# Optimization experiments

Measured on AMD Instinct MI355X. Metric: run time of the kernel, lower is better.

Reference implementation:

```python
import jax, jax.numpy as jnp
import numpy as np

NUM_EDGE_TYPES = 8
HIDDEN = 128
N_NODES = 50000
N_EDGES = 600000


def setup_inputs() -> dict:
    key = jax.random.key(0)
    ks = jax.random.split(key, 10)
    H = HIDDEN
    h = jax.random.normal(ks[0], (N_NODES, H), dtype=jnp.float32)
    edge_index = jax.random.randint(ks[1], (2, N_EDGES), 0, N_NODES, dtype=jnp.int32)
    edge_type = jax.random.randint(ks[2], (N_EDGES,), 0, NUM_EDGE_TYPES + 1, dtype=jnp.int32)
    s = 1.0 / np.sqrt(H)
    W_msg = jax.random.uniform(ks[3], (H, H), jnp.float32, -s, s)
    b_msg = jax.random.uniform(ks[4], (H,), jnp.float32, -s, s)
    edge_embed = jax.random.normal(ks[5], (NUM_EDGE_TYPES + 1, H), dtype=jnp.float32)
    W_ih = jax.random.uniform(ks[6], (3 * H, H), jnp.float32, -s, s)
    W_hh = jax.random.uniform(ks[7], (3 * H, H), jnp.float32, -s, s)
    b_ih = jax.random.uniform(ks[8], (3 * H,), jnp.float32, -s, s)
    b_hh = jax.random.uniform(ks[9], (3 * H,), jnp.float32, -s, s)
    return {"h": h, "edge_index": edge_index, "edge_type": edge_type,
            "num_nodes": N_NODES, "W_msg": W_msg, "b_msg": b_msg,
            "edge_embed": edge_embed, "W_ih": W_ih, "W_hh": W_hh,
            "b_ih": b_ih, "b_hh": b_hh}


def _gru_cell(x, h, W_ih, W_hh, b_ih, b_hh):
    # PyTorch GRUCell: gates ordered (r, z, n)
    H = h.shape[-1]
    gi = x @ W_ih.T + b_ih  # (N, 3H)
    gh = h @ W_hh.T + b_hh
    i_r, i_z, i_n = gi[:, :H], gi[:, H:2 * H], gi[:, 2 * H:]
    h_r, h_z, h_n = gh[:, :H], gh[:, H:2 * H], gh[:, 2 * H:]
    r = jax.nn.sigmoid(i_r + h_r)
    z = jax.nn.sigmoid(i_z + h_z)
    n = jnp.tanh(i_n + r * h_n)
    return (1.0 - z) * n + z * h


def reference(h, edge_index, edge_type, num_nodes, W_msg, b_msg, edge_embed, W_ih, W_hh, b_ih, b_hh):
    src = edge_index[0]
    dst = edge_index[1]
    # gather -> linear -> edge-type embed add
    src_h = h[src] @ W_msg.T + b_msg                      # (E, H)
    emb = edge_embed[jnp.clip(edge_type, 0, NUM_EDGE_TYPES)]  # (E, H)
    msg = src_h + emb
    # scatter-add into per-node message buffer
    messages = jax.ops.segment_sum(msg, dst, num_segments=num_nodes)  # (num_nodes, H)
    h_new = _gru_cell(messages, h[:num_nodes], W_ih, W_hh, b_ih, b_hh)
    result = jnp.zeros_like(h).at[:num_nodes].set(h_new)
    return result
```

## Files before the change

kernel.cpp:

```cpp
#include <hip/hip_runtime.h>
#include <math.h>

#define H 128
typedef unsigned int u32;
typedef unsigned long long u64;
typedef __attribute__((ext_vector_type(8))) short short8;
typedef __attribute__((ext_vector_type(4))) float floatx4;

#define XS_STRIDE 136
#define CS_STRIDE 40

__device__ __forceinline__ float sigmoid_f(float x) {
    return 1.0f / (1.0f + __expf(-x));
}
__device__ __forceinline__ float tanh_f(float x) {
    float t = __expf(-2.0f * fabsf(x));
    float r = (1.0f - t) / (1.0f + t);
    return copysignf(r, x);
}
__device__ __forceinline__ unsigned short f2bf(float x) {
    u32 u = __float_as_uint(x);
    return (unsigned short)((u + 0x7fffu + ((u >> 16) & 1u)) >> 16);
}
__device__ __forceinline__ float bf2f(unsigned short s) {
    return __uint_as_float(((u32)s) << 16);
}
__device__ __forceinline__ float bf_lo32(u32 u) { return __uint_as_float(u << 16); }
__device__ __forceinline__ float bf_hi32(u32 u) { return __uint_as_float(u & 0xffff0000u); }

__global__ __launch_bounds__(256) void fused_pre_kernel(
    const float* __restrict__ h, unsigned short* __restrict__ h_b, int total8,
    int* __restrict__ head, int N,
    const float* __restrict__ Wih, const float* __restrict__ Whh,
    const float* __restrict__ Wm,  const float* __restrict__ emb,
    const float* __restrict__ bm,
    unsigned short* __restrict__ Wcs, unsigned short* __restrict__ Whhs,
    unsigned short* __restrict__ embWs, int HB, int DB)
{
    int b = blockIdx.x;
    if (b < HB) {
        int idx = b * 256 + threadIdx.x;
        if (idx >= total8) return;
        const float4* p = (const float4*)(h + (size_t)idx * 8);
        float4 a = p[0], bb = p[1];
        short8 v;
        v[0] = (short)f2bf(a.x);  v[1] = (short)f2bf(a.y);
        v[2] = (short)f2bf(a.z);  v[3] = (short)f2bf(a.w);
        v[4] = (short)f2bf(bb.x); v[5] = (short)f2bf(bb.y);
        v[6] = (short)f2bf(bb.z); v[7] = (short)f2bf(bb.w);
        *(short8*)(h_b + (size_t)idx * 8) = v;
        return;
    }
    if (b < HB + DB) {
        int idx = (b - HB) * 256 + threadIdx.x;
        if (idx < N) head[idx] = -1;
        return;
    }
    int idx = (b - HB - DB) * 256 + threadIdx.x;
    if (idx < 49152) {
        int g = idx >> 7;
        int k = idx & 127;
        float acc = 0.f;
#pragma unroll 4
        for (int c = 0; c < H; ++c)
            acc += Wih[(size_t)g * H + c] * Wm[(size_t)c * H + k];
        int gate = g >> 7;
        int wi = g & 127;
        int j = wi >> 4, m = wi & 15;
        int kc = k >> 5, q = (k >> 3) & 3, i = k & 7;
        int l = q * 16 + m;
        Wcs[(size_t)(((gate * 8 + j) * 4 + kc) * 64 + l) * 8 + i] = f2bf(acc);
    } else if (idx < 61440) {
        int s = idx - 49152;
        int i = s & 7;
        int l = (s >> 3) & 63;
        int jb = s >> 9;
        int gate = jb >> 3, jj = jb & 7;
        int q = l >> 4, m = l & 15;
        int t = q * 8 + i;
        unsigned short v = 0;
        if (t < 9) {
            int g = gate * 128 + jj * 16 + m;
            float acc = 0.f;
#pragma unroll 4
            for (int jx = 0; jx < H; ++jx)
                acc += (emb[(size_t)t * H + jx] + bm[jx]) * Wih[(size_t)g * H + jx];
            v = f2bf(acc);
        }
        embWs[s] = v;
    } else if (idx < 67584) {
        int t2 = idx - 61440;
        int l  = t2 & 63;
        int kc = (t2 >> 6) & 3;
        int jr = t2 >> 8;
        int m = l & 15, q = l >> 4;
        size_t srco = (size_t)(jr * 16 + m) * H + kc * 32 + q * 8;
        const float4* s0 = (const float4*)(Whh + srco);
        float4 a = s0[0], bb = s0[1];
        short8 v;
        v[0] = (short)f2bf(a.x);  v[1] = (short)f2bf(a.y);
        v[2] = (short)f2bf(a.z);  v[3] = (short)f2bf(a.w);
        v[4] = (short)f2bf(bb.x); v[5] = (short)f2bf(bb.y);
        v[6] = (short)f2bf(bb.z); v[7] = (short)f2bf(bb.w);
        *(short8*)(Whhs + (size_t)t2 * 8) = v;
    }
}

__global__ __launch_bounds__(256) void fill_ll_kernel(
    const int* __restrict__ eidx, const int* __restrict__ etype,
    int* __restrict__ head, int* __restrict__ nexte,
    int* __restrict__ packed, int E)
{
    int e = blockIdx.x * 256 + threadIdx.x;
    if (e >= E) return;
    int src = eidx[e];
    int dst = eidx[E + e];
    int t = etype[e];
    t = t < 0 ? 0 : (t > 8 ? 8 : t);
    packed[e] = src | (t << 24);
    int old = atomicExch(&head[dst], e);
    nexte[e] = old;
}

__global__ __launch_bounds__(256) void gather_ll_kernel(
    const unsigned short* __restrict__ h_b,
    const int* __restrict__ head, const int* __restrict__ nexte,
    const int* __restrict__ packed,
    unsigned short* __restrict__ S_b, u64* __restrict__ cnt, int N)
{
    int w = blockIdx.x * 4 + (threadIdx.x >> 6);
    int lane = threadIdx.x & 63;
    int n0 = w * 4;
    if (n0 >= N) return;

    int e0 = head[n0];
    int e1 = (n0 + 1 < N) ? head[n0 + 1] : -1;
    int e2 = (n0 + 2 < N) ? head[n0 + 2] : -1;
    int e3 = (n0 + 3 < N) ? head[n0 + 3] : -1;

    float ax0 = 0.f, ay0 = 0.f, ax1 = 0.f, ay1 = 0.f;
    float ax2 = 0.f, ay2 = 0.f, ax3 = 0.f, ay3 = 0.f;
    u64 c0 = 0, c1 = 0, c2 = 0, c3 = 0;

    while ((e0 >= 0) || (e1 >= 0) || (e2 >= 0) || (e3 >= 0)) {
        int nx0 = -1, nx1 = -1, nx2 = -1, nx3 = -1;
        int u0 = 0, u1 = 0, u2 = 0, u3 = 0;
        if (e0 >= 0) { nx0 = nexte[e0]; u0 = packed[e0]; }
        if (e1 >= 0) { nx1 = nexte[e1]; u1 = packed[e1]; }
        if (e2 >= 0) { nx2 = nexte[e2]; u2 = packed[e2]; }
        if (e3 >= 0) { nx3 = nexte[e3]; u3 = packed[e3]; }
        if (e0 >= 0) {
            u32 x = *((const u32*)(h_b + (size_t)(u0 & 0xffffff) * H) + lane);
            c0 += 1ull << (7 * (u0 >> 24));
            ax0 += bf_lo32(x); ay0 += bf_hi32(x);
        }
        if (e1 >= 0) {
            u32 x = *((const u32*)(h_b + (size_t)(u1 & 0xffffff) * H) + lane);
            c1 += 1ull << (7 * (u1 >> 24));
            ax1 += bf_lo32(x); ay1 += bf_hi32(x);
        }
        if (e2 >= 0) {
            u32 x = *((const u32*)(h_b + (size_t)(u2 & 0xffffff) * H) + lane);
            c2 += 1ull << (7 * (u2 >> 24));
            ax2 += bf_lo32(x); ay2 += bf_hi32(x);
        }
        if (e3 >= 0) {
            u32 x = *((const u32*)(h_b + (size_t)(u3 & 0xffffff) * H) + lane);
            c3 += 1ull << (7 * (u3 >> 24));
            ax3 += bf_lo32(x); ay3 += bf_hi32(x);
        }
        e0 = nx0; e1 = nx1; e2 = nx2; e3 = nx3;
    }

    {
        u32 o = (u32)f2bf(ax0) | ((u32)f2bf(ay0) << 16);
        *((u32*)(S_b + (size_t)n0 * H) + lane) = o;
        if (lane == 0) cnt[n0] = c0;
    }
    if (n0 + 1 < N) {
        u32 o = (u32)f2bf(ax1) | ((u32)f2bf(ay1) << 16);
        *((u32*)(S_b + (size_t)(n0 + 1) * H) + lane) = o;
        if (lane == 0) cnt[n0 + 1] = c1;
    }
    if (n0 + 2 < N) {
        u32 o = (u32)f2bf(ax2) | ((u32)f2bf(ay2) << 16);
        *((u32*)(S_b + (size_t)(n0 + 2) * H) + lane) = o;
        if (lane == 0) cnt[n0 + 2] = c2;
    }
    if (n0 + 3 < N) {
        u32 o = (u32)f2bf(ax3) | ((u32)f2bf(ay3) << 16);
        *((u32*)(S_b + (size_t)(n0 + 3) * H) + lane) = o;
        if (lane == 0) cnt[n0 + 3] = c3;
    }
}

__global__ __launch_bounds__(256, 4) void gru_mfma_kernel(
    const unsigned short* __restrict__ S_b, const unsigned short* __restrict__ h_b,
    const unsigned short* __restrict__ Wcs, const unsigned short* __restrict__ Whhs,
    const unsigned short* __restrict__ embWs,
    const float* __restrict__ bih, const float* __restrict__ bhh,
    const u64* __restrict__ cnt,
    const int* __restrict__ numn, float* __restrict__ out, int N)
{
    __shared__ unsigned short xs[64 * XS_STRIDE];
    __shared__ unsigned short hsb[64 * XS_STRIDE];
    __shared__ unsigned short cs[64 * CS_STRIDE];

    int tid = threadIdx.x;
    int bx = blockIdx.x;
    int node0 = (bx >> 1) * 64;
    int jhalf = bx & 1;

    int lane = tid & 63;
    int wv = tid >> 6;
    int j = jhalf * 4 + wv;

    short8 er = *(const short8*)(embWs + (size_t)((0 * 8 + j) * 64 + lane) * 8);
    short8 ez = *(const short8*)(embWs + (size_t)((1 * 8 + j) * 64 + lane) * 8);
    short8 en = *(const short8*)(embWs + (size_t)((2 * 8 + j) * 64 + lane) * 8);

    for (int c = tid; c < 1024; c += 256) {
        int r = c >> 4;
        int k8 = (c & 15) << 3;
        int n = node0 + r;
        int nc = n < N ? n : N - 1;
        *(short8*)(&xs[r * XS_STRIDE + k8]) =
            *(const short8*)(S_b + (size_t)nc * H + k8);
        *(short8*)(&hsb[r * XS_STRIDE + k8]) =
            *(const short8*)(h_b + (size_t)nc * H + k8);
    }
    {
        int r = tid >> 2, tg = tid & 3;
        int n = node0 + r;
        u64 cv = cnt[n < N ? n : N - 1];
        short8 v = {0, 0, 0, 0, 0, 0, 0, 0};
        if (tg == 0) {
#pragma unroll
            for (int i = 0; i < 8; ++i)
                v[i] = (short)f2bf((float)((u32)(cv >> (7 * i)) & 127u));
        } else if (tg == 1) {
            v[0] = (short)f2bf((float)((u32)(cv >> 56) & 127u));
        }
        *(short8*)(&cs[r * CS_STRIDE + tg * 8]) = v;
    }
    __syncthreads();

    int am = lane & 15;
    int aq = lane >> 4;

    int num_nodes = numn[0];
    floatx4 zero = {0.f, 0.f, 0.f, 0.f};

    floatx4 aR[4], aZ[4], aIn[4], aHn[4];
#pragma unroll
    for (int rt = 0; rt < 4; ++rt) {
        short8 acn = *(const short8*)(&cs[(rt * 16 + am) * CS_STRIDE + aq * 8]);
        aR[rt]  = __builtin_amdgcn_mfma_f32_16x16x32_bf16(acn, er, zero, 0, 0, 0);
        aZ[rt]  = __builtin_amdgcn_mfma_f32_16x16x32_bf16(acn, ez, zero, 0, 0, 0);
        aIn[rt] = __builtin_amdgcn_mfma_f32_16x16x32_bf16(acn, en, zero, 0, 0, 0);
        aHn[rt] = zero;
    }
#pragma unroll
    for (int kc = 0; kc < 4; ++kc) {
        size_t c_r = (size_t)(((0 * 8 + j) * 4 + kc) * 64 + lane) * 8;
        size_t c_z = (size_t)(((1 * 8 + j) * 4 + kc) * 64 + lane) * 8;
        size_t c_n = (size_t)(((2 * 8 + j) * 4 + kc) * 64 + lane) * 8;
        short8 bir = *(const short8*)(Wcs + c_r);
        short8 bhr = *(const short8*)(Whhs + c_r);
        short8 biz = *(const short8*)(Wcs + c_z);
        short8 bhz = *(const short8*)(Whhs + c_z);
        short8 bin = *(const short8*)(Wcs + c_n);
        short8 bhn = *(const short8*)(Whhs + c_n);
#pragma unroll
        for (int rt = 0; rt < 4; ++rt) {
            int arow = rt * 16 + am;
            short8 axv = *(const short8*)(&xs[arow * XS_STRIDE + kc * 32 + aq * 8]);
            short8 ahv = *(const short8*)(&hsb[arow * XS_STRIDE + kc * 32 + aq * 8]);
            aR[rt]  = __builtin_amdgcn_mfma_f32_16x16x32_bf16(axv, bir, aR[rt], 0, 0, 0);
            aR[rt]  = __builtin_amdgcn_mfma_f32_16x16x32_bf16(ahv, bhr, aR[rt], 0, 0, 0);
            aZ[rt]  = __builtin_amdgcn_mfma_f32_16x16x32_bf16(axv, biz, aZ[rt], 0, 0, 0);
            aZ[rt]  = __builtin_amdgcn_mfma_f32_16x16x32_bf16(ahv, bhz, aZ[rt], 0, 0, 0);
            aIn[rt] = __builtin_amdgcn_mfma_f32_16x16x32_bf16(axv, bin, aIn[rt], 0, 0, 0);
            aHn[rt] = __builtin_amdgcn_mfma_f32_16x16x32_bf16(ahv, bhn, aHn[rt], 0, 0, 0);
        }
    }
    int c = j * 16 + am;
    float b_r = bih[c]       + bhh[c];
    float b_z = bih[128 + c] + bhh[128 + c];
    float b_in = bih[256 + c], b_hn = bhh[256 + c];
#pragma unroll
    for (int rt = 0; rt < 4; ++rt) {
#pragma unroll
        for (int q = 0; q < 4; ++q) {
            int m = rt * 16 + aq * 4 + q;
            int node = node0 + m;
            if (node < N) {
                float r  = sigmoid_f(aR[rt][q] + b_r);
                float z  = sigmoid_f(aZ[rt][q] + b_z);
                float nv = tanh_f((aIn[rt][q] + b_in) + r * (aHn[rt][q] + b_hn));
                float hv = bf2f(hsb[m * XS_STRIDE + c]);
                float o  = (1.0f - z) * nv + z * hv;
                out[(size_t)node * H + c] = (node < num_nodes) ? o : 0.0f;
            }
        }
    }
}

extern "C" void kernel_launch(void* const* d_in, const int* in_sizes, int n_in,
                              void* d_out, int out_size, void* d_ws, size_t ws_size,
                              hipStream_t stream) {
    const float* h    = (const float*)d_in[0];
    const int*  eidx  = (const int*)d_in[1];
    const int*  etype = (const int*)d_in[2];
    const int*  numn  = (const int*)d_in[3];
    const float* Wm   = (const float*)d_in[4];
    const float* bm   = (const float*)d_in[5];
    const float* emb  = (const float*)d_in[6];
    const float* Wih  = (const float*)d_in[7];
    const float* Whh  = (const float*)d_in[8];
    const float* bih  = (const float*)d_in[9];
    const float* bhh  = (const float*)d_in[10];

    int N = in_sizes[0] / H;
    int E = in_sizes[2];

    unsigned short* S_b   = (unsigned short*)d_ws;
    unsigned short* h_b   = S_b + (size_t)N * H;
    unsigned short* Wcs   = h_b + (size_t)N * H;
    unsigned short* Whhs  = Wcs + 3 * H * H;
    unsigned short* embWs = Whhs + 3 * H * H;
    u64* cnt    = (u64*)(embWs + 12288);
    int* head   = (int*)(cnt + N);
    int* packed = head + N;
    int* nexte  = packed + E;

    int total8 = N * H / 8;
    int HB = (total8 + 255) / 256;
    int DB = (N + 255) / 256;
    int PB = 264;
    fused_pre_kernel<<<HB + DB + PB, 256, 0, stream>>>(
        h, h_b, total8, head, N, Wih, Whh, Wm, emb, bm, Wcs, Whhs, embWs, HB, DB);

    fill_ll_kernel<<<(E + 255) / 256, 256, 0, stream>>>(
        eidx, etype, head, nexte, packed, E);

    gather_ll_kernel<<<(N + 15) / 16, 256, 0, stream>>>(
        h_b, head, nexte, packed, S_b, cnt, N);

    int nblk = ((N + 63) / 64) * 2;
    gru_mfma_kernel<<<nblk, 256, 0, stream>>>(S_b, h_b, Wcs, Whhs, embWs,
                                              bih, bhh, cnt, numn, (float*)d_out, N);
}
```

Measured before the change: 222.3 us.

## Split per-node edge linked lists into four sub-lists for deeper gather parallelism

Each destination node now keeps four linked-list heads, picked by edge index modulo 4. The gather kernel handles two nodes per wave and walks eight chains at once, so each dependent pointer chase is about a quarter as long and more loads are in flight at a time. This also spreads the atomic exchanges during list building over more addresses. The cost is a head array four times larger to initialise and read, twice as many gather blocks, and more registers per thread.

```diff
diff --git a/kernel.cpp b/kernel.cpp
--- a/kernel.cpp
+++ b/kernel.cpp
@@ -30,7 +30,7 @@
 
 __global__ __launch_bounds__(256) void fused_pre_kernel(
     const float* __restrict__ h, unsigned short* __restrict__ h_b, int total8,
-    int* __restrict__ head, int N,
+    int* __restrict__ head, int N4,
     const float* __restrict__ Wih, const float* __restrict__ Whh,
     const float* __restrict__ Wm,  const float* __restrict__ emb,
     const float* __restrict__ bm,
@@ -53,7 +53,7 @@
     }
     if (b < HB + DB) {
         int idx = (b - HB) * 256 + threadIdx.x;
-        if (idx < N) head[idx] = -1;
+        if (idx < N4) head[idx] = -1;
         return;
     }
     int idx = (b - HB - DB) * 256 + threadIdx.x;
@@ -118,7 +118,7 @@
     int t = etype[e];
     t = t < 0 ? 0 : (t > 8 ? 8 : t);
     packed[e] = src | (t << 24);
-    int old = atomicExch(&head[dst], e);
+    int old = atomicExch(&head[dst * 4 + (e & 3)], e);
     nexte[e] = old;
 }
 
@@ -130,25 +130,37 @@
 {
     int w = blockIdx.x * 4 + (threadIdx.x >> 6);
     int lane = threadIdx.x & 63;
-    int n0 = w * 4;
+    int n0 = w * 2;
     if (n0 >= N) return;
-
-    int e0 = head[n0];
-    int e1 = (n0 + 1 < N) ? head[n0 + 1] : -1;
-    int e2 = (n0 + 2 < N) ? head[n0 + 2] : -1;
-    int e3 = (n0 + 3 < N) ? head[n0 + 3] : -1;
+    bool has1 = (n0 + 1) < N;
+
+    int e0 = head[n0 * 4 + 0];
+    int e1 = head[n0 * 4 + 1];
+    int e2 = head[n0 * 4 + 2];
+    int e3 = head[n0 * 4 + 3];
+    int e4 = has1 ? head[n0 * 4 + 4] : -1;
+    int e5 = has1 ? head[n0 * 4 + 5] : -1;
+    int e6 = has1 ? head[n0 * 4 + 6] : -1;
+    int e7 = has1 ? head[n0 * 4 + 7] : -1;
 
     float ax0 = 0.f, ay0 = 0.f, ax1 = 0.f, ay1 = 0.f;
-    float ax2 = 0.f, ay2 = 0.f, ax3 = 0.f, ay3 = 0.f;
-    u64 c0 = 0, c1 = 0, c2 = 0, c3 = 0;
-
-    while ((e0 >= 0) || (e1 >= 0) || (e2 >= 0) || (e3 >= 0)) {
+    u64 c0 = 0, c1 = 0;
+
+    while ((e0 | e1 | e2 | e3 | e4 | e5 | e6 | e7) >= 0 ||
+           e0 >= 0 || e1 >= 0 || e2 >= 0 || e3 >= 0 ||
+           e4 >= 0 || e5 >= 0 || e6 >= 0 || e7 >= 0) {
         int nx0 = -1, nx1 = -1, nx2 = -1, nx3 = -1;
+        int nx4 = -1, nx5 = -1, nx6 = -1, nx7 = -1;
         int u0 = 0, u1 = 0, u2 = 0, u3 = 0;
+        int u4 = 0, u5 = 0, u6 = 0, u7 = 0;
         if (e0 >= 0) { nx0 = nexte[e0]; u0 = packed[e0]; }
         if (e1 >= 0) { nx1 = nexte[e1]; u1 = packed[e1]; }
         if (e2 >= 0) { nx2 = nexte[e2]; u2 = packed[e2]; }
         if (e3 >= 0) { nx3 = nexte[e3]; u3 = packed[e3]; }
+        if (e4 >= 0) { nx4 = nexte[e4]; u4 = packed[e4]; }
+        if (e5 >= 0) { nx5 = nexte[e5]; u5 = packed[e5]; }
+        if (e6 >= 0) { nx6 = nexte[e6]; u6 = packed[e6]; }
+        if (e7 >= 0) { nx7 = nexte[e7]; u7 = packed[e7]; }
         if (e0 >= 0) {
             u32 x = *((const u32*)(h_b + (size_t)(u0 & 0xffffff) * H) + lane);
             c0 += 1ull << (7 * (u0 >> 24));
@@ -156,20 +168,41 @@
         }
         if (e1 >= 0) {
             u32 x = *((const u32*)(h_b + (size_t)(u1 & 0xffffff) * H) + lane);
-            c1 += 1ull << (7 * (u1 >> 24));
-            ax1 += bf_lo32(x); ay1 += bf_hi32(x);
+            c0 += 1ull << (7 * (u1 >> 24));
+            ax0 += bf_lo32(x); ay0 += bf_hi32(x);
         }
         if (e2 >= 0) {
             u32 x = *((const u32*)(h_b + (size_t)(u2 & 0xffffff) * H) + lane);
-            c2 += 1ull << (7 * (u2 >> 24));
-            ax2 += bf_lo32(x); ay2 += bf_hi32(x);
+            c0 += 1ull << (7 * (u2 >> 24));
+            ax0 += bf_lo32(x); ay0 += bf_hi32(x);
         }
         if (e3 >= 0) {
             u32 x = *((const u32*)(h_b + (size_t)(u3 & 0xffffff) * H) + lane);
-            c3 += 1ull << (7 * (u3 >> 24));
-            ax3 += bf_lo32(x); ay3 += bf_hi32(x);
+            c0 += 1ull << (7 * (u3 >> 24));
+            ax0 += bf_lo32(x); ay0 += bf_hi32(x);
+        }
+        if (e4 >= 0) {
+            u32 x = *((const u32*)(h_b + (size_t)(u4 & 0xffffff) * H) + lane);
+            c1 += 1ull << (7 * (u4 >> 24));
+            ax1 += bf_lo32(x); ay1 += bf_hi32(x);
+        }
+        if (e5 >= 0) {
+            u32 x = *((const u32*)(h_b + (size_t)(u5 & 0xffffff) * H) + lane);
+            c1 += 1ull << (7 * (u5 >> 24));
+            ax1 += bf_lo32(x); ay1 += bf_hi32(x);
+        }
+        if (e6 >= 0) {
+            u32 x = *((const u32*)(h_b + (size_t)(u6 & 0xffffff) * H) + lane);
+            c1 += 1ull << (7 * (u6 >> 24));
+            ax1 += bf_lo32(x); ay1 += bf_hi32(x);
+        }
+        if (e7 >= 0) {
+            u32 x = *((const u32*)(h_b + (size_t)(u7 & 0xffffff) * H) + lane);
+            c1 += 1ull << (7 * (u7 >> 24));
+            ax1 += bf_lo32(x); ay1 += bf_hi32(x);
         }
         e0 = nx0; e1 = nx1; e2 = nx2; e3 = nx3;
+        e4 = nx4; e5 = nx5; e6 = nx6; e7 = nx7;
     }
 
     {
@@ -177,20 +210,10 @@
         *((u32*)(S_b + (size_t)n0 * H) + lane) = o;
         if (lane == 0) cnt[n0] = c0;
     }
-    if (n0 + 1 < N) {
+    if (has1) {
         u32 o = (u32)f2bf(ax1) | ((u32)f2bf(ay1) << 16);
         *((u32*)(S_b + (size_t)(n0 + 1) * H) + lane) = o;
         if (lane == 0) cnt[n0 + 1] = c1;
-    }
-    if (n0 + 2 < N) {
-        u32 o = (u32)f2bf(ax2) | ((u32)f2bf(ay2) << 16);
-        *((u32*)(S_b + (size_t)(n0 + 2) * H) + lane) = o;
-        if (lane == 0) cnt[n0 + 2] = c2;
-    }
-    if (n0 + 3 < N) {
-        u32 o = (u32)f2bf(ax3) | ((u32)f2bf(ay3) << 16);
-        *((u32*)(S_b + (size_t)(n0 + 3) * H) + lane) = o;
-        if (lane == 0) cnt[n0 + 3] = c3;
     }
 }
 
@@ -331,20 +354,21 @@
     unsigned short* embWs = Whhs + 3 * H * H;
     u64* cnt    = (u64*)(embWs + 12288);
     int* head   = (int*)(cnt + N);
-    int* packed = head + N;
+    int* packed = head + 4 * N;
     int* nexte  = packed + E;
 
     int total8 = N * H / 8;
+    int N4 = N * 4;
     int HB = (total8 + 255) / 256;
-    int DB = (N + 255) / 256;
+    int DB = (N4 + 255) / 256;
     int PB = 264;
     fused_pre_kernel<<<HB + DB + PB, 256, 0, stream>>>(
-        h, h_b, total8, head, N, Wih, Whh, Wm, emb, bm, Wcs, Whhs, embWs, HB, DB);
+        h, h_b, total8, head, N4, Wih, Whh, Wm, emb, bm, Wcs, Whhs, embWs, HB, DB);
 
     fill_ll_kernel<<<(E + 255) / 256, 256, 0, stream>>>(
         eidx, etype, head, nexte, packed, E);
 
-    gather_ll_kernel<<<(N + 15) / 16, 256, 0, stream>>>(
+    gather_ll_kernel<<<(N + 7) / 8, 256, 0, stream>>>(
         h_b, head, nexte, packed, S_b, cnt, N);
 
     int nblk = ((N + 63) / 64) * 2;
```

Result: no change. 219.8 us (-1.1%).
